# Kernel tuning notes

Hardware: AMD Instinct MI355X
Metric: run time of the kernel (lower is better)

## Reference

```python
import jax, jax.numpy as jnp
import numpy as np

EPS = 1e-12  # matches torch F.normalize eps


def _l2norm(x, axis):
    n = jnp.sqrt(jnp.sum(x * x, axis=axis, keepdims=True))
    return x / jnp.maximum(n, EPS)


def _avg_pool(x, k):
    # x: [B, C, H, W], H and W divisible by k
    B, C, H, W = x.shape
    return x.reshape(B, C, H // k, k, W // k, k).mean(axis=(3, 5))


def setup_inputs() -> dict:
    key = jax.random.key(0)
    k1, k2, k3, k4 = jax.random.split(key, 4)
    B, N, C = 4, 256, 256
    Hp, Wp = 96, 128
    return {
        "q_t": jax.random.normal(k1, (B, N, C), dtype=jnp.float32),
        "f_t": jax.random.normal(k2, (B, Hp * Wp, C), dtype=jnp.float32),
        "w1": jax.random.normal(k3, (16, 4, 3, 3), dtype=jnp.float32) * 0.1,
        "w2": jax.random.normal(k4, (1, 16, 3, 3), dtype=jnp.float32) * 0.1,
        "H_prime": 96,
        "W_prime": 128,
    }


def reference(q_t, f_t, w1, w2, H_prime, W_prime):
    B, N, C = q_t.shape
    qn = _l2norm(q_t, axis=-1)  # [B, N, C]
    # f_t: [B, P, C] -> [B, C, H', W']
    f = f_t.reshape(B, H_prime, W_prime, C).transpose(0, 3, 1, 2)
    cs = []
    for i in range(4):  # pyramid levels, pool kernel 1/2/4/8
        k = 1 << i
        fl = f if k == 1 else _avg_pool(f, k)
        h, w = H_prime // k, W_prime // k
        fln = _l2norm(fl.reshape(B, C, h * w), axis=1)  # normalize over channels
        c = jnp.einsum('bnc,bcp->bnp', qn, fln)  # [B, N, h*w]
        c = c.reshape(B * N, 1, h, w)
        if k > 1:
            # torch bilinear align_corners=False == half-pixel linear resize
            c = jax.image.resize(c, (B * N, 1, H_prime, W_prime), method='linear')
        cs.append(c)
    c = jnp.concatenate(cs, axis=1)  # [B*N, 4, H', W']
    # cnn_corr branch: conv3x3 -> relu -> conv3x3, residual with level-0 corr
    hmid = jax.lax.conv_general_dilated(c, w1, (1, 1), 'SAME')
    hmid = jax.nn.relu(hmid)
    out = jax.lax.conv_general_dilated(hmid, w2, (1, 1), 'SAME') + c[:, 0:1]
    return out.reshape(B, N, H_prime * W_prime)
```

## Files before the change

### kernel.cpp

```cpp
#include <hip/hip_runtime.h>
#include <hip/hip_fp16.h>

#define BB 4
#define NN 256
#define CC 256
#define HH 96
#define WW 128
#define P0 (HH*WW)
#define TOTPOS 16320

#define SH 16
#define SW 64
#define CTH 20
#define CTW 68
#define HMH 18
#define HMW 66

typedef _Float16 f16x4 __attribute__((ext_vector_type(4)));
typedef _Float16 f16x8 __attribute__((ext_vector_type(8)));
typedef _Float16 h2    __attribute__((ext_vector_type(2)));
typedef float    f32x4 __attribute__((ext_vector_type(4)));

#if defined(__has_builtin)
#if __has_builtin(__builtin_amdgcn_fdot2)
#define FDOT2(a,b,c) __builtin_amdgcn_fdot2((a),(b),(c),false)
#endif
#endif
#ifndef FDOT2
#define FDOT2(a,b,c) ((c) + (float)(a)[0]*(float)(b)[0] + (float)(a)[1]*(float)(b)[1])
#endif

union F4U { f16x4 v; uint2 u; };
union F8U { f16x8 v; uint4 u; h2 h[4]; };

__device__ __forceinline__ int hm_swz(int hx) {
    return (hx & 0xC) << 2;
}

__global__ __launch_bounds__(64) void k_prep(const float* __restrict__ w1,
                                             _Float16* __restrict__ bfT) {
    int lane = threadIdx.x;
    int oc = lane & 15, og = lane >> 4;
    f16x8 bf0, bf1;
    #pragma unroll
    for (int e = 0; e < 8; ++e) {
        int k0 = og * 8 + e;
        bf0[e] = (_Float16)w1[oc * 36 + (k0 & 3) * 9 + (k0 >> 2)];
        int k1 = 32 + og * 8 + e;
        int kk1 = k1 >> 2;
        bf1[e] = (kk1 <= 8) ? (_Float16)w1[oc * 36 + (k1 & 3) * 9 + kk1] : (_Float16)0.f;
    }
    *(f16x8*)(bfT + lane * 16)     = bf0;
    *(f16x8*)(bfT + lane * 16 + 8) = bf1;
}

__global__ __launch_bounds__(256) void k_qnorm(const float* __restrict__ q,
                                               _Float16* __restrict__ qn16) {
    int wid = blockIdx.x * 4 + (threadIdx.x >> 6);
    int lane = threadIdx.x & 63;
    const float4* src = (const float4*)(q + (size_t)wid * CC);
    float4 v = src[lane];
    float ss = v.x*v.x + v.y*v.y + v.z*v.z + v.w*v.w;
    #pragma unroll
    for (int off = 32; off > 0; off >>= 1) ss += __shfl_xor(ss, off, 64);
    float inv = 1.0f / fmaxf(sqrtf(ss), 1e-12f);
    f16x4 o;
    o[0] = (_Float16)(v.x*inv); o[1] = (_Float16)(v.y*inv);
    o[2] = (_Float16)(v.z*inv); o[3] = (_Float16)(v.w*inv);
    *(f16x4*)(qn16 + (size_t)wid * CC + lane * 4) = o;
}

__global__ __launch_bounds__(256) void k_pool_norm(const float* __restrict__ f,
                                                   _Float16* __restrict__ flnT) {
    int b = blockIdx.y;
    int gp = blockIdx.x;
    int lvl, pos;
    if (gp < 12288)      { lvl = 0; pos = gp; }
    else if (gp < 15360) { lvl = 1; pos = gp - 12288; }
    else if (gp < 16128) { lvl = 2; pos = gp - 15360; }
    else                 { lvl = 3; pos = gp - 16128; }
    int k = 1 << lvl;
    int wl = WW >> lvl;
    int py = pos / wl, px = pos - py * wl;
    int c = threadIdx.x;
    int iy0 = py * k, ix0 = px * k;
    float sum = 0.f;
    for (int dy = 0; dy < k; ++dy)
        for (int dx = 0; dx < k; ++dx) {
            int ip = (iy0 + dy) * WW + ix0 + dx;
            sum += f[((size_t)b * P0 + ip) * CC + c];
        }
    float val = sum * (1.0f / (float)(k * k));
    float ss = val * val;
    #pragma unroll
    for (int off = 32; off > 0; off >>= 1) ss += __shfl_xor(ss, off, 64);
    __shared__ float red[4];
    __shared__ float s_inv;
    if ((threadIdx.x & 63) == 0) red[threadIdx.x >> 6] = ss;
    __syncthreads();
    if (threadIdx.x == 0) {
        float t = red[0] + red[1] + red[2] + red[3];
        s_inv = 1.0f / fmaxf(sqrtf(t), 1e-12f);
    }
    __syncthreads();
    flnT[((size_t)b * TOTPOS + gp) * CC + c] = (_Float16)(val * s_inv);
}

__global__ __launch_bounds__(256, 4) void k_gemm(const _Float16* __restrict__ qn16,
                                                 const _Float16* __restrict__ flnT,
                                                 float* __restrict__ cws) {
    int b = blockIdx.z;
    int wv = threadIdx.x >> 6, lane = threadIdx.x & 63;
    int m0 = blockIdx.y * 64 + (wv >> 1) * 32;
    int p0 = blockIdx.x * 64 + (wv & 1) * 32;
    int r = lane & 15, og = lane >> 4;

    const f16x8* A0p = (const f16x8*)(qn16 + ((size_t)(b * NN + m0 + r)) * CC) + og;
    const f16x8* A1p = (const f16x8*)(qn16 + ((size_t)(b * NN + m0 + 16 + r)) * CC) + og;
    const f16x8* B0p = (const f16x8*)(flnT + ((size_t)b * TOTPOS + p0 + r) * CC) + og;
    const f16x8* B1p = (const f16x8*)(flnT + ((size_t)b * TOTPOS + p0 + 16 + r) * CC) + og;

    f32x4 acc00 = {0,0,0,0}, acc01 = {0,0,0,0}, acc10 = {0,0,0,0}, acc11 = {0,0,0,0};
    #pragma unroll 4
    for (int ko = 0; ko < 8; ++ko) {
        f16x8 a0 = A0p[ko * 4];
        f16x8 a1 = A1p[ko * 4];
        f16x8 b0 = B0p[ko * 4];
        f16x8 b1 = B1p[ko * 4];
        acc00 = __builtin_amdgcn_mfma_f32_16x16x32_f16(a0, b0, acc00, 0, 0, 0);
        acc01 = __builtin_amdgcn_mfma_f32_16x16x32_f16(a0, b1, acc01, 0, 0, 0);
        acc10 = __builtin_amdgcn_mfma_f32_16x16x32_f16(a1, b0, acc10, 0, 0, 0);
        acc11 = __builtin_amdgcn_mfma_f32_16x16x32_f16(a1, b1, acc11, 0, 0, 0);
    }
    size_t rowBase = (size_t)(b * NN + m0 + og * 4) * TOTPOS;
    #pragma unroll
    for (int rr = 0; rr < 4; ++rr) {
        size_t ro0 = rowBase + (size_t)rr * TOTPOS;
        size_t ro1 = ro0 + (size_t)16 * TOTPOS;
        cws[ro0 + p0 + r]      = acc00[rr];
        cws[ro0 + p0 + 16 + r] = acc01[rr];
        cws[ro1 + p0 + r]      = acc10[rr];
        cws[ro1 + p0 + 16 + r] = acc11[rr];
    }
}

__global__ __launch_bounds__(512, 6) void k_fuse(const float* __restrict__ cws,
                                                 const _Float16* __restrict__ bfT,
                                                 const float* __restrict__ w2,
                                                 float* __restrict__ out) {
    __shared__ _Float16 cT[CTH * CTW * 4];
    __shared__ _Float16 hm[HMH * HMW * 16];
    __shared__ h2 w2h2[72];
    __shared__ int   xt01[3][CTW];
    __shared__ float xttx[3][CTW];
    __shared__ int   yt01[3][CTH];
    __shared__ float ytty[3][CTH];
    int img   = blockIdx.y;
    int strip = blockIdx.x;
    int y0 = (strip >> 1) * SH;
    int x0 = (strip & 1) * SW;
    int tid = threadIdx.x;
    int lane = tid & 63, wv = tid >> 6;
    int oc = lane & 15, og = lane >> 4;
    const float* cb = cws + (size_t)img * TOTPOS;

    if (tid < 72) {
        int tap = tid >> 3, j = tid & 7;
        h2 w; w[0] = (_Float16)w2[(2 * j) * 9 + tap];
        w[1] = (_Float16)w2[(2 * j + 1) * 9 + tap];
        w2h2[tid] = w;
    }
    for (int i = tid; i < 3 * CTW; i += 512) {
        int l = i / CTW + 1, rx = i - (l - 1) * CTW;
        int wl = WW >> l;
        float invk = (l == 1) ? 0.5f : (l == 2) ? 0.25f : 0.125f;
        float fx = ((x0 + rx - 2) + 0.5f) * invk - 0.5f;
        float x0f = floorf(fx);
        int ix = (int)x0f;
        int x1 = min(ix + 1, wl - 1); if (x1 < 0) x1 = 0;
        int xc = min(max(ix, 0), wl - 1);
        xt01[l - 1][rx] = xc | (x1 << 16);
        xttx[l - 1][rx] = fx - x0f;
    }
    if (tid < 3 * CTH) {
        int l = tid / CTH + 1, ry = tid - (l - 1) * CTH;
        int hl = HH >> l;
        float invk = (l == 1) ? 0.5f : (l == 2) ? 0.25f : 0.125f;
        float fy = ((y0 + ry - 2) + 0.5f) * invk - 0.5f;
        float y0f = floorf(fy);
        int iy = (int)y0f;
        int y1 = min(iy + 1, hl - 1); if (y1 < 0) y1 = 0;
        int yc = min(max(iy, 0), hl - 1);
        yt01[l - 1][ry] = yc | (y1 << 16);
        ytty[l - 1][ry] = fy - y0f;
    }

    f16x8 bf0 = *(const f16x8*)(bfT + lane * 16);
    f16x8 bf1 = *(const f16x8*)(bfT + lane * 16 + 8);
    int ofs0, ofs1, ofs8;
    {
        int kk0 = 2 * og,     ky0 = kk0 / 3, kx0 = kk0 - ky0 * 3;
        int kk1 = 2 * og + 1, ky1 = kk1 / 3, kx1 = kk1 - ky1 * 3;
        ofs0 = (ky0 * CTW + kx0 + 1 + oc) * 4;
        ofs1 = (ky1 * CTW + kx1 + 1 + oc) * 4;
        ofs8 = (2 * CTW + 2 + 1 + oc) * 4;
    }
    {
        uint4 z; z.x = z.y = z.z = z.w = 0u;
        uint4* hp = (uint4*)hm;
        for (int i = tid; i < (HMH * HMW * 16 * 2) / 16; i += 512) hp[i] = z;
    }
    __syncthreads();

    for (int i = tid; i < CTH * CTW; i += 512) {
        int ry = i / CTW, rx = i - ry * CTW;
        int gy = y0 + ry - 2, gx = x0 + rx - 2;
        f16x4 vv = {(_Float16)0.f, (_Float16)0.f, (_Float16)0.f, (_Float16)0.f};
        if ((unsigned)gy < HH && (unsigned)gx < WW) {
            vv[0] = (_Float16)cb[gy * WW + gx];
            #pragma unroll
            for (int l = 1; l < 4; ++l) {
                int wl = WW >> l;
                int lvlOff = (l == 1) ? 12288 : (l == 2) ? 15360 : 16128;
                int p01 = xt01[l - 1][rx];
                float tx = xttx[l - 1][rx];
                int q01 = yt01[l - 1][ry];
                float ty = ytty[l - 1][ry];
                int xa = p01 & 0xFFFF, xb = p01 >> 16;
                int ya = q01 & 0xFFFF, yb = q01 >> 16;
                const float* r0 = cb + lvlOff + ya * wl;
                const float* r1 = cb + lvlOff + yb * wl;
                float v00 = r0[xa], v01 = r0[xb];
                float v10 = r1[xa], v11 = r1[xb];
                float top = v00 + tx * (v01 - v00);
                float bot = v10 + tx * (v11 - v10);
                vv[l] = (_Float16)(top + ty * (bot - top));
            }
        }
        *(f16x4*)&cT[i * 4] = vv;
    }
    __syncthreads();

    for (int it = 0; it < 12; ++it) {
        int t = it * 8 + wv;
        if (t >= 90) break;
        int hyr = t / 5, xg = t - hyr * 5;
        if ((unsigned)(y0 + hyr - 1) >= (unsigned)HH) continue;
        int xb = (xg < 4) ? xg * 16 - 1 : 49;
        int base = (hyr * CTW + xb) * 4;
        F4U a00, a01, a8;
        a00.v = *(const f16x4*)&cT[base + ofs0];
        a01.v = *(const f16x4*)&cT[base + ofs1];
        a8.v  = *(const f16x4*)&cT[base + ofs8];
        F8U A0, A1;
        A0.u.x = a00.u.x; A0.u.y = a00.u.y; A0.u.z = a01.u.x; A0.u.w = a01.u.y;
        A1.u.x = a8.u.x;  A1.u.y = a8.u.y;  A1.u.z = a8.u.x;  A1.u.w = a8.u.y;
        f32x4 acc = {0.f, 0.f, 0.f, 0.f};
        acc = __builtin_amdgcn_mfma_f32_16x16x32_f16(A0.v, bf0, acc, 0, 0, 0);
        acc = __builtin_amdgcn_mfma_f32_16x16x32_f16(A1.v, bf1, acc, 0, 0, 0);
        int hxb = xb + og * 4 + 1;
        #pragma unroll
        for (int r = 0; r < 4; ++r) {
            int hx = hxb + r;
            int imgx = x0 + hx - 1;
            bool st = ((unsigned)imgx < (unsigned)WW) && (xg < 4 || hx >= 64);
            if (st) {
                int byt = ((hyr * HMW + hx) * 32 + oc * 2) ^ hm_swz(hx);
                *(_Float16*)((char*)hm + byt) = (_Float16)fmaxf(acc[r], 0.f);
            }
        }
    }
    __syncthreads();

    int row = tid >> 5, x2 = (tid & 31) * 2;
    int colof[4][2];
    #pragma unroll
    for (int c4 = 0; c4 < 4; ++c4) {
        int hx = x2 + c4;
        int sw = hm_swz(hx);
        colof[c4][0] = (hx * 32) ^ sw;
        colof[c4][1] = (hx * 32 + 16) ^ sw;
    }
    float a2[2] = {0.f, 0.f};
    #pragma unroll
    for (int r = 0; r < 3; ++r) {
        int rowb = (row + r) * (HMW * 32);
        h2 wrow[3][8];
        #pragma unroll
        for (int kx = 0; kx < 3; ++kx)
            #pragma unroll
            for (int j = 0; j < 8; ++j) wrow[kx][j] = w2h2[(r * 3 + kx) * 8 + j];
        F8U d[4][2];
        #pragma unroll
        for (int c4 = 0; c4 < 4; ++c4) {
            d[c4][0].v = *(const f16x8*)((const char*)hm + (rowb + colof[c4][0]));
            d[c4][1].v = *(const f16x8*)((const char*)hm + (rowb + colof[c4][1]));
        }
        #pragma unroll
        for (int q = 0; q < 2; ++q)
            #pragma unroll
            for (int kx = 0; kx < 3; ++kx) {
                #pragma unroll
                for (int j = 0; j < 4; ++j) {
                    a2[q] = FDOT2(d[q + kx][0].h[j], wrow[kx][j], a2[q]);
                    a2[q] = FDOT2(d[q + kx][1].h[j], wrow[kx][j + 4], a2[q]);
                }
            }
    }
    int gy = y0 + row, gx = x0 + x2;
    const float2 res = *(const float2*)&cb[gy * WW + gx];
    float2 o;
    o.x = a2[0] + res.x; o.y = a2[1] + res.y;
    *(float2*)&out[(size_t)img * P0 + gy * WW + gx] = o;
}

extern "C" void kernel_launch(void* const* d_in, const int* in_sizes, int n_in,
                              void* d_out, int out_size, void* d_ws, size_t ws_size,
                              hipStream_t stream) {
    const float* q  = (const float*)d_in[0];
    const float* f  = (const float*)d_in[1];
    const float* w1 = (const float*)d_in[2];
    const float* w2 = (const float*)d_in[3];
    float* out = (float*)d_out;

    float* cws = (float*)d_ws;
    _Float16* flnT = (_Float16*)(cws + (size_t)BB * NN * TOTPOS);
    _Float16* qn16 = flnT + (size_t)BB * TOTPOS * CC;
    _Float16* bfT  = qn16 + (size_t)BB * NN * CC;

    hipLaunchKernelGGL(k_prep, dim3(1), dim3(64), 0, stream, w1, bfT);
    hipLaunchKernelGGL(k_qnorm, dim3(BB * NN / 4), dim3(256), 0, stream, q, qn16);
    hipLaunchKernelGGL(k_pool_norm, dim3(TOTPOS, BB), dim3(256), 0, stream, f, flnT);
    hipLaunchKernelGGL(k_gemm, dim3(255, 4, BB), dim3(256), 0, stream, qn16, flnT, cws);
    hipLaunchKernelGGL(k_fuse, dim3(12, BB * NN), dim3(512), 0, stream, cws, bfT, w2, out);
}
```

Baseline: 345.9 us.

## Store correlation in fp16 and precompute bilinear upsampled levels in separate kernel

The GEMM now writes the correlation workspace in fp16 instead of fp32, halving that write traffic. A new kernel performs the bilinear upsampling of the three pooled levels once per image into three full-resolution fp16 buffers, so the fused conv kernel loads four values per pixel instead of recomputing the interpolation with gathers in every overlapping tile. The residual is taken from the shared-memory tile rather than reloaded from global memory. The trade-off is three extra full-resolution buffers (about 3x 25MB) that must be written and read back, plus an extra launch, and fp16 rounding of the residual term.

```diff
diff --git a/kernel.cpp b/kernel.cpp
--- a/kernel.cpp
+++ b/kernel.cpp
@@ -108,7 +108,7 @@
 
 __global__ __launch_bounds__(256, 4) void k_gemm(const _Float16* __restrict__ qn16,
                                                  const _Float16* __restrict__ flnT,
-                                                 float* __restrict__ cws) {
+                                                 _Float16* __restrict__ cws16) {
     int b = blockIdx.z;
     int wv = threadIdx.x >> 6, lane = threadIdx.x & 63;
     int m0 = blockIdx.y * 64 + (wv >> 1) * 32;
@@ -137,24 +137,57 @@
     for (int rr = 0; rr < 4; ++rr) {
         size_t ro0 = rowBase + (size_t)rr * TOTPOS;
         size_t ro1 = ro0 + (size_t)16 * TOTPOS;
-        cws[ro0 + p0 + r]      = acc00[rr];
-        cws[ro0 + p0 + 16 + r] = acc01[rr];
-        cws[ro1 + p0 + r]      = acc10[rr];
-        cws[ro1 + p0 + 16 + r] = acc11[rr];
-    }
-}
-
-__global__ __launch_bounds__(512, 6) void k_fuse(const float* __restrict__ cws,
+        cws16[ro0 + p0 + r]      = (_Float16)acc00[rr];
+        cws16[ro0 + p0 + 16 + r] = (_Float16)acc01[rr];
+        cws16[ro1 + p0 + r]      = (_Float16)acc10[rr];
+        cws16[ro1 + p0 + 16 + r] = (_Float16)acc11[rr];
+    }
+}
+
+__global__ __launch_bounds__(256) void k_upsample(const _Float16* __restrict__ cws16,
+                                                  _Float16* __restrict__ cu1,
+                                                  _Float16* __restrict__ cu2,
+                                                  _Float16* __restrict__ cu3) {
+    int img = blockIdx.y;
+    int p = blockIdx.x * 256 + threadIdx.x;
+    int y = p >> 7, x = p & 127;
+    const _Float16* cb = cws16 + (size_t)img * TOTPOS;
+    _Float16 r[3];
+    #pragma unroll
+    for (int l = 1; l < 4; ++l) {
+        int hl = HH >> l, wl = WW >> l;
+        int lvlOff = (l == 1) ? 12288 : (l == 2) ? 15360 : 16128;
+        float invk = (l == 1) ? 0.5f : (l == 2) ? 0.25f : 0.125f;
+        float fy = (y + 0.5f) * invk - 0.5f;
+        float fx = (x + 0.5f) * invk - 0.5f;
+        float y0f = floorf(fy), x0f = floorf(fx);
+        float ty = fy - y0f, tx = fx - x0f;
+        int iy = (int)y0f, ix = (int)x0f;
+        int y1 = min(iy + 1, hl - 1);
+        iy = min(max(iy, 0), hl - 1);
+        int x1 = min(ix + 1, wl - 1);
+        ix = min(max(ix, 0), wl - 1);
+        const _Float16* base = cb + lvlOff;
+        float v00 = (float)base[iy * wl + ix], v01 = (float)base[iy * wl + x1];
+        float v10 = (float)base[y1 * wl + ix], v11 = (float)base[y1 * wl + x1];
+        float top = v00 + tx * (v01 - v00);
+        float bot = v10 + tx * (v11 - v10);
+        r[l - 1] = (_Float16)(top + ty * (bot - top));
+    }
+    size_t o = (size_t)img * P0 + p;
+    cu1[o] = r[0]; cu2[o] = r[1]; cu3[o] = r[2];
+}
+
+__global__ __launch_bounds__(512, 6) void k_fuse(const _Float16* __restrict__ cws16,
+                                                 const _Float16* __restrict__ cu1,
+                                                 const _Float16* __restrict__ cu2,
+                                                 const _Float16* __restrict__ cu3,
                                                  const _Float16* __restrict__ bfT,
                                                  const float* __restrict__ w2,
                                                  float* __restrict__ out) {
     __shared__ _Float16 cT[CTH * CTW * 4];
     __shared__ _Float16 hm[HMH * HMW * 16];
     __shared__ h2 w2h2[72];
-    __shared__ int   xt01[3][CTW];
-    __shared__ float xttx[3][CTW];
-    __shared__ int   yt01[3][CTH];
-    __shared__ float ytty[3][CTH];
     int img   = blockIdx.y;
     int strip = blockIdx.x;
     int y0 = (strip >> 1) * SH;
@@ -162,37 +195,14 @@
     int tid = threadIdx.x;
     int lane = tid & 63, wv = tid >> 6;
     int oc = lane & 15, og = lane >> 4;
-    const float* cb = cws + (size_t)img * TOTPOS;
+    const _Float16* cb16 = cws16 + (size_t)img * TOTPOS;
+    size_t ib = (size_t)img * P0;
 
     if (tid < 72) {
         int tap = tid >> 3, j = tid & 7;
         h2 w; w[0] = (_Float16)w2[(2 * j) * 9 + tap];
         w[1] = (_Float16)w2[(2 * j + 1) * 9 + tap];
         w2h2[tid] = w;
-    }
-    for (int i = tid; i < 3 * CTW; i += 512) {
-        int l = i / CTW + 1, rx = i - (l - 1) * CTW;
-        int wl = WW >> l;
-        float invk = (l == 1) ? 0.5f : (l == 2) ? 0.25f : 0.125f;
-        float fx = ((x0 + rx - 2) + 0.5f) * invk - 0.5f;
-        float x0f = floorf(fx);
-        int ix = (int)x0f;
-        int x1 = min(ix + 1, wl - 1); if (x1 < 0) x1 = 0;
-        int xc = min(max(ix, 0), wl - 1);
-        xt01[l - 1][rx] = xc | (x1 << 16);
-        xttx[l - 1][rx] = fx - x0f;
-    }
-    if (tid < 3 * CTH) {
-        int l = tid / CTH + 1, ry = tid - (l - 1) * CTH;
-        int hl = HH >> l;
-        float invk = (l == 1) ? 0.5f : (l == 2) ? 0.25f : 0.125f;
-        float fy = ((y0 + ry - 2) + 0.5f) * invk - 0.5f;
-        float y0f = floorf(fy);
-        int iy = (int)y0f;
-        int y1 = min(iy + 1, hl - 1); if (y1 < 0) y1 = 0;
-        int yc = min(max(iy, 0), hl - 1);
-        yt01[l - 1][ry] = yc | (y1 << 16);
-        ytty[l - 1][ry] = fy - y0f;
     }
 
     f16x8 bf0 = *(const f16x8*)(bfT + lane * 16);
@@ -210,32 +220,16 @@
         uint4* hp = (uint4*)hm;
         for (int i = tid; i < (HMH * HMW * 16 * 2) / 16; i += 512) hp[i] = z;
     }
-    __syncthreads();
-
     for (int i = tid; i < CTH * CTW; i += 512) {
         int ry = i / CTW, rx = i - ry * CTW;
         int gy = y0 + ry - 2, gx = x0 + rx - 2;
         f16x4 vv = {(_Float16)0.f, (_Float16)0.f, (_Float16)0.f, (_Float16)0.f};
         if ((unsigned)gy < HH && (unsigned)gx < WW) {
-            vv[0] = (_Float16)cb[gy * WW + gx];
-            #pragma unroll
-            for (int l = 1; l < 4; ++l) {
-                int wl = WW >> l;
-                int lvlOff = (l == 1) ? 12288 : (l == 2) ? 15360 : 16128;
-                int p01 = xt01[l - 1][rx];
-                float tx = xttx[l - 1][rx];
-                int q01 = yt01[l - 1][ry];
-                float ty = ytty[l - 1][ry];
-                int xa = p01 & 0xFFFF, xb = p01 >> 16;
-                int ya = q01 & 0xFFFF, yb = q01 >> 16;
-                const float* r0 = cb + lvlOff + ya * wl;
-                const float* r1 = cb + lvlOff + yb * wl;
-                float v00 = r0[xa], v01 = r0[xb];
-                float v10 = r1[xa], v11 = r1[xb];
-                float top = v00 + tx * (v01 - v00);
-                float bot = v10 + tx * (v11 - v10);
-                vv[l] = (_Float16)(top + ty * (bot - top));
-            }
+            int gp = gy * WW + gx;
+            vv[0] = cb16[gp];
+            vv[1] = cu1[ib + gp];
+            vv[2] = cu2[ib + gp];
+            vv[3] = cu3[ib + gp];
         }
         *(f16x4*)&cT[i * 4] = vv;
     }
@@ -308,9 +302,10 @@
             }
     }
     int gy = y0 + row, gx = x0 + x2;
-    const float2 res = *(const float2*)&cb[gy * WW + gx];
+    float r0 = (float)cT[((row + 2) * CTW + (x2 + 2)) * 4];
+    float r1 = (float)cT[((row + 2) * CTW + (x2 + 3)) * 4];
     float2 o;
-    o.x = a2[0] + res.x; o.y = a2[1] + res.y;
+    o.x = a2[0] + r0; o.y = a2[1] + r1;
     *(float2*)&out[(size_t)img * P0 + gy * WW + gx] = o;
 }
 
@@ -323,14 +318,20 @@
     const float* w2 = (const float*)d_in[3];
     float* out = (float*)d_out;
 
-    float* cws = (float*)d_ws;
-    _Float16* flnT = (_Float16*)(cws + (size_t)BB * NN * TOTPOS);
+    _Float16* wsh  = (_Float16*)d_ws;
+    _Float16* cws16 = wsh;
+    _Float16* cu1  = cws16 + (size_t)BB * NN * TOTPOS;
+    _Float16* cu2  = cu1 + (size_t)BB * NN * P0;
+    _Float16* cu3  = cu2 + (size_t)BB * NN * P0;
+    _Float16* flnT = cu3 + (size_t)BB * NN * P0;
     _Float16* qn16 = flnT + (size_t)BB * TOTPOS * CC;
     _Float16* bfT  = qn16 + (size_t)BB * NN * CC;
 
     hipLaunchKernelGGL(k_prep, dim3(1), dim3(64), 0, stream, w1, bfT);
     hipLaunchKernelGGL(k_qnorm, dim3(BB * NN / 4), dim3(256), 0, stream, q, qn16);
     hipLaunchKernelGGL(k_pool_norm, dim3(TOTPOS, BB), dim3(256), 0, stream, f, flnT);
-    hipLaunchKernelGGL(k_gemm, dim3(255, 4, BB), dim3(256), 0, stream, qn16, flnT, cws);
-    hipLaunchKernelGGL(k_fuse, dim3(12, BB * NN), dim3(512), 0, stream, cws, bfT, w2, out);
-}
+    hipLaunchKernelGGL(k_gemm, dim3(255, 4, BB), dim3(256), 0, stream, qn16, flnT, cws16);
+    hipLaunchKernelGGL(k_upsample, dim3(48, BB * NN), dim3(256), 0, stream, cws16, cu1, cu2, cu3);
+    hipLaunchKernelGGL(k_fuse, dim3(12, BB * NN), dim3(512), 0, stream,
+                       cws16, cu1, cu2, cu3, bfT, w2, out);
+}
```

Result: slower. 362.1 us (+4.7%).

## Store correlation workspace in fp16 and trim conv epilogue overheads

Applied to the files above, without the earlier changes.

The GEMM now writes the correlation volume as fp16 instead of fp32, so the write traffic and the gathered reads in the fuse kernel are halved. The residual add now reads the level-0 value from the shared-memory tile instead of global memory. The hidden-layer store branches are specialised to drop per-element bounds checks, and the w2 weights are loaded as 16-byte vectors. The cost is extra fp16 rounding of the correlation before bilinear interpolation and in the residual path, which may reduce accuracy.

```diff
diff --git a/kernel.cpp b/kernel.cpp
--- a/kernel.cpp
+++ b/kernel.cpp
@@ -108,7 +108,7 @@
 
 __global__ __launch_bounds__(256, 4) void k_gemm(const _Float16* __restrict__ qn16,
                                                  const _Float16* __restrict__ flnT,
-                                                 float* __restrict__ cws) {
+                                                 _Float16* __restrict__ cws16) {
     int b = blockIdx.z;
     int wv = threadIdx.x >> 6, lane = threadIdx.x & 63;
     int m0 = blockIdx.y * 64 + (wv >> 1) * 32;
@@ -137,14 +137,14 @@
     for (int rr = 0; rr < 4; ++rr) {
         size_t ro0 = rowBase + (size_t)rr * TOTPOS;
         size_t ro1 = ro0 + (size_t)16 * TOTPOS;
-        cws[ro0 + p0 + r]      = acc00[rr];
-        cws[ro0 + p0 + 16 + r] = acc01[rr];
-        cws[ro1 + p0 + r]      = acc10[rr];
-        cws[ro1 + p0 + 16 + r] = acc11[rr];
-    }
-}
-
-__global__ __launch_bounds__(512, 6) void k_fuse(const float* __restrict__ cws,
+        cws16[ro0 + p0 + r]      = (_Float16)acc00[rr];
+        cws16[ro0 + p0 + 16 + r] = (_Float16)acc01[rr];
+        cws16[ro1 + p0 + r]      = (_Float16)acc10[rr];
+        cws16[ro1 + p0 + 16 + r] = (_Float16)acc11[rr];
+    }
+}
+
+__global__ __launch_bounds__(512, 6) void k_fuse(const _Float16* __restrict__ cws16,
                                                  const _Float16* __restrict__ bfT,
                                                  const float* __restrict__ w2,
                                                  float* __restrict__ out) {
@@ -162,7 +162,7 @@
     int tid = threadIdx.x;
     int lane = tid & 63, wv = tid >> 6;
     int oc = lane & 15, og = lane >> 4;
-    const float* cb = cws + (size_t)img * TOTPOS;
+    const _Float16* cb16 = cws16 + (size_t)img * TOTPOS;
 
     if (tid < 72) {
         int tap = tid >> 3, j = tid & 7;
@@ -217,7 +217,7 @@
         int gy = y0 + ry - 2, gx = x0 + rx - 2;
         f16x4 vv = {(_Float16)0.f, (_Float16)0.f, (_Float16)0.f, (_Float16)0.f};
         if ((unsigned)gy < HH && (unsigned)gx < WW) {
-            vv[0] = (_Float16)cb[gy * WW + gx];
+            vv[0] = cb16[gy * WW + gx];
             #pragma unroll
             for (int l = 1; l < 4; ++l) {
                 int wl = WW >> l;
@@ -228,10 +228,10 @@
                 float ty = ytty[l - 1][ry];
                 int xa = p01 & 0xFFFF, xb = p01 >> 16;
                 int ya = q01 & 0xFFFF, yb = q01 >> 16;
-                const float* r0 = cb + lvlOff + ya * wl;
-                const float* r1 = cb + lvlOff + yb * wl;
-                float v00 = r0[xa], v01 = r0[xb];
-                float v10 = r1[xa], v11 = r1[xb];
+                const _Float16* r0 = cb16 + lvlOff + ya * wl;
+                const _Float16* r1 = cb16 + lvlOff + yb * wl;
+                float v00 = (float)r0[xa], v01 = (float)r0[xb];
+                float v10 = (float)r1[xa], v11 = (float)r1[xb];
                 float top = v00 + tx * (v01 - v00);
                 float bot = v10 + tx * (v11 - v10);
                 vv[l] = (_Float16)(top + ty * (bot - top));
@@ -259,14 +259,33 @@
         acc = __builtin_amdgcn_mfma_f32_16x16x32_f16(A0.v, bf0, acc, 0, 0, 0);
         acc = __builtin_amdgcn_mfma_f32_16x16x32_f16(A1.v, bf1, acc, 0, 0, 0);
         int hxb = xb + og * 4 + 1;
-        #pragma unroll
-        for (int r = 0; r < 4; ++r) {
-            int hx = hxb + r;
-            int imgx = x0 + hx - 1;
-            bool st = ((unsigned)imgx < (unsigned)WW) && (xg < 4 || hx >= 64);
-            if (st) {
-                int byt = ((hyr * HMW + hx) * 32 + oc * 2) ^ hm_swz(hx);
-                *(_Float16*)((char*)hm + byt) = (_Float16)fmaxf(acc[r], 0.f);
+        if (xg < 4) {
+            if (x0 == 0 && xg == 0) {
+                #pragma unroll
+                for (int r = 0; r < 4; ++r) {
+                    int hx = hxb + r;
+                    if (hx > 0) {
+                        int byt = ((hyr * HMW + hx) * 32 + oc * 2) ^ hm_swz(hx);
+                        *(_Float16*)((char*)hm + byt) = (_Float16)fmaxf(acc[r], 0.f);
+                    }
+                }
+            } else {
+                #pragma unroll
+                for (int r = 0; r < 4; ++r) {
+                    int hx = hxb + r;
+                    int byt = ((hyr * HMW + hx) * 32 + oc * 2) ^ hm_swz(hx);
+                    *(_Float16*)((char*)hm + byt) = (_Float16)fmaxf(acc[r], 0.f);
+                }
+            }
+        } else {
+            #pragma unroll
+            for (int r = 0; r < 4; ++r) {
+                int hx = hxb + r;
+                int imgx = x0 + hx - 1;
+                if (hx >= 64 && (unsigned)imgx < (unsigned)WW) {
+                    int byt = ((hyr * HMW + hx) * 32 + oc * 2) ^ hm_swz(hx);
+                    *(_Float16*)((char*)hm + byt) = (_Float16)fmaxf(acc[r], 0.f);
+                }
             }
         }
     }
@@ -285,11 +304,12 @@
     #pragma unroll
     for (int r = 0; r < 3; ++r) {
         int rowb = (row + r) * (HMW * 32);
-        h2 wrow[3][8];
-        #pragma unroll
-        for (int kx = 0; kx < 3; ++kx)
+        F8U ww[6];
+        {
+            const f16x8* wp = (const f16x8*)(w2h2 + r * 24);
             #pragma unroll
-            for (int j = 0; j < 8; ++j) wrow[kx][j] = w2h2[(r * 3 + kx) * 8 + j];
+            for (int j = 0; j < 6; ++j) ww[j].v = wp[j];
+        }
         F8U d[4][2];
         #pragma unroll
         for (int c4 = 0; c4 < 4; ++c4) {
@@ -302,15 +322,18 @@
             for (int kx = 0; kx < 3; ++kx) {
                 #pragma unroll
                 for (int j = 0; j < 4; ++j) {
-                    a2[q] = FDOT2(d[q + kx][0].h[j], wrow[kx][j], a2[q]);
-                    a2[q] = FDOT2(d[q + kx][1].h[j], wrow[kx][j + 4], a2[q]);
+                    int fi0 = kx * 8 + j;
+                    int fi1 = kx * 8 + j + 4;
+                    a2[q] = FDOT2(d[q + kx][0].h[j], ww[fi0 >> 2].h[fi0 & 3], a2[q]);
+                    a2[q] = FDOT2(d[q + kx][1].h[j], ww[fi1 >> 2].h[fi1 & 3], a2[q]);
                 }
             }
     }
     int gy = y0 + row, gx = x0 + x2;
-    const float2 res = *(const float2*)&cb[gy * WW + gx];
+    float r0 = (float)cT[((row + 2) * CTW + (x2 + 2)) * 4];
+    float r1 = (float)cT[((row + 2) * CTW + (x2 + 3)) * 4];
     float2 o;
-    o.x = a2[0] + res.x; o.y = a2[1] + res.y;
+    o.x = a2[0] + r0; o.y = a2[1] + r1;
     *(float2*)&out[(size_t)img * P0 + gy * WW + gx] = o;
 }
 
@@ -323,14 +346,15 @@
     const float* w2 = (const float*)d_in[3];
     float* out = (float*)d_out;
 
-    float* cws = (float*)d_ws;
-    _Float16* flnT = (_Float16*)(cws + (size_t)BB * NN * TOTPOS);
-    _Float16* qn16 = flnT + (size_t)BB * TOTPOS * CC;
-    _Float16* bfT  = qn16 + (size_t)BB * NN * CC;
+    _Float16* wsh   = (_Float16*)d_ws;
+    _Float16* cws16 = wsh;
+    _Float16* flnT  = cws16 + (size_t)BB * NN * TOTPOS;
+    _Float16* qn16  = flnT + (size_t)BB * TOTPOS * CC;
+    _Float16* bfT   = qn16 + (size_t)BB * NN * CC;
 
     hipLaunchKernelGGL(k_prep, dim3(1), dim3(64), 0, stream, w1, bfT);
     hipLaunchKernelGGL(k_qnorm, dim3(BB * NN / 4), dim3(256), 0, stream, q, qn16);
     hipLaunchKernelGGL(k_pool_norm, dim3(TOTPOS, BB), dim3(256), 0, stream, f, flnT);
-    hipLaunchKernelGGL(k_gemm, dim3(255, 4, BB), dim3(256), 0, stream, qn16, flnT, cws);
-    hipLaunchKernelGGL(k_fuse, dim3(12, BB * NN), dim3(512), 0, stream, cws, bfT, w2, out);
-}
+    hipLaunchKernelGGL(k_gemm, dim3(255, 4, BB), dim3(256), 0, stream, qn16, flnT, cws16);
+    hipLaunchKernelGGL(k_fuse, dim3(12, BB * NN), dim3(512), 0, stream, cws16, bfT, w2, out);
+}
```

Result: slower. 360.1 us (+4.1%).

## Compute all pyramid levels per 8x8 tile in one pass over features

Applied to the files above, without the earlier changes.

The pooling/normalization kernel now gives each block an 8x8 spatial tile. The block loads the tile into shared memory once as fp16, builds the 2x2, 4x4 and 8x8 pooled levels hierarchically, and computes per-position channel norms cooperatively before writing all levels. Before, every level re-read the full fp32 feature map, so the input was read about four times; now it is read once, and the launch drops from 16320 tiny blocks to 192 per batch. The trade-off is about 45 KB of shared memory per block, which limits occupancy. Storing raw features in fp16 before pooling and normalizing also adds slight rounding differences.

```diff
diff --git a/kernel.cpp b/kernel.cpp
--- a/kernel.cpp
+++ b/kernel.cpp
@@ -72,38 +72,99 @@
 
 __global__ __launch_bounds__(256) void k_pool_norm(const float* __restrict__ f,
                                                    _Float16* __restrict__ flnT) {
+    __shared__ _Float16 vals[64][258];
+    __shared__ _Float16 pooled[21][258];
+    __shared__ float part_ss[256];
+    __shared__ float inv_norm[85];
     int b = blockIdx.y;
-    int gp = blockIdx.x;
-    int lvl, pos;
-    if (gp < 12288)      { lvl = 0; pos = gp; }
-    else if (gp < 15360) { lvl = 1; pos = gp - 12288; }
-    else if (gp < 16128) { lvl = 2; pos = gp - 15360; }
-    else                 { lvl = 3; pos = gp - 16128; }
-    int k = 1 << lvl;
-    int wl = WW >> lvl;
-    int py = pos / wl, px = pos - py * wl;
+    int tile = blockIdx.x;
+    int ty = tile >> 4, tx = tile & 15;
     int c = threadIdx.x;
-    int iy0 = py * k, ix0 = px * k;
-    float sum = 0.f;
-    for (int dy = 0; dy < k; ++dy)
-        for (int dx = 0; dx < k; ++dx) {
-            int ip = (iy0 + dy) * WW + ix0 + dx;
-            sum += f[((size_t)b * P0 + ip) * CC + c];
+
+    const float* fb = f + ((size_t)b * P0) * CC + c;
+    #pragma unroll 4
+    for (int p = 0; p < 64; ++p) {
+        int py = p >> 3, px = p & 7;
+        int ip = (ty * 8 + py) * WW + tx * 8 + px;
+        vals[p][c] = (_Float16)fb[(size_t)ip * CC];
+    }
+    __syncthreads();
+
+    #pragma unroll
+    for (int p1 = 0; p1 < 16; ++p1) {
+        int py = p1 >> 2, px = p1 & 3;
+        float s = (float)vals[(2*py)*8 + 2*px][c]     + (float)vals[(2*py)*8 + 2*px + 1][c]
+                + (float)vals[(2*py+1)*8 + 2*px][c]   + (float)vals[(2*py+1)*8 + 2*px + 1][c];
+        pooled[p1][c] = (_Float16)(s * 0.25f);
+    }
+    #pragma unroll
+    for (int p2 = 0; p2 < 4; ++p2) {
+        int py = p2 >> 1, px = p2 & 1;
+        float s = (float)pooled[(2*py)*4 + 2*px][c]   + (float)pooled[(2*py)*4 + 2*px + 1][c]
+                + (float)pooled[(2*py+1)*4 + 2*px][c] + (float)pooled[(2*py+1)*4 + 2*px + 1][c];
+        pooled[16 + p2][c] = (_Float16)(s * 0.25f);
+    }
+    {
+        float s = (float)pooled[16][c] + (float)pooled[17][c]
+                + (float)pooled[18][c] + (float)pooled[19][c];
+        pooled[20][c] = (_Float16)(s * 0.25f);
+    }
+    __syncthreads();
+
+    {
+        int pos = c >> 2, part = c & 3;
+        float ss = 0.f;
+        const _Float16* vp = &vals[pos][part * 64];
+        #pragma unroll 8
+        for (int j = 0; j < 64; ++j) { float v = (float)vp[j]; ss += v * v; }
+        part_ss[c] = ss;
+    }
+    __syncthreads();
+    if (c < 64) {
+        float t = part_ss[4*c] + part_ss[4*c+1] + part_ss[4*c+2] + part_ss[4*c+3];
+        inv_norm[c] = 1.0f / fmaxf(sqrtf(t), 1e-12f);
+    }
+    __syncthreads();
+    {
+        int pos = c >> 2, part = c & 3;
+        float ss = 0.f;
+        if (pos < 21) {
+            const _Float16* vp = &pooled[pos][part * 64];
+            #pragma unroll 8
+            for (int j = 0; j < 64; ++j) { float v = (float)vp[j]; ss += v * v; }
         }
-    float val = sum * (1.0f / (float)(k * k));
-    float ss = val * val;
-    #pragma unroll
-    for (int off = 32; off > 0; off >>= 1) ss += __shfl_xor(ss, off, 64);
-    __shared__ float red[4];
-    __shared__ float s_inv;
-    if ((threadIdx.x & 63) == 0) red[threadIdx.x >> 6] = ss;
-    __syncthreads();
-    if (threadIdx.x == 0) {
-        float t = red[0] + red[1] + red[2] + red[3];
-        s_inv = 1.0f / fmaxf(sqrtf(t), 1e-12f);
-    }
-    __syncthreads();
-    flnT[((size_t)b * TOTPOS + gp) * CC + c] = (_Float16)(val * s_inv);
+        part_ss[c] = ss;
+    }
+    __syncthreads();
+    if (c < 21) {
+        float t = part_ss[4*c] + part_ss[4*c+1] + part_ss[4*c+2] + part_ss[4*c+3];
+        inv_norm[64 + c] = 1.0f / fmaxf(sqrtf(t), 1e-12f);
+    }
+    __syncthreads();
+
+    size_t base = (size_t)b * TOTPOS;
+    #pragma unroll 4
+    for (int p = 0; p < 64; ++p) {
+        int py = p >> 3, px = p & 7;
+        int gp = (ty * 8 + py) * WW + tx * 8 + px;
+        flnT[(base + gp) * CC + c] = (_Float16)((float)vals[p][c] * inv_norm[p]);
+    }
+    #pragma unroll
+    for (int p1 = 0; p1 < 16; ++p1) {
+        int py = p1 >> 2, px = p1 & 3;
+        int gp = 12288 + (ty * 4 + py) * 64 + tx * 4 + px;
+        flnT[(base + gp) * CC + c] = (_Float16)((float)pooled[p1][c] * inv_norm[64 + p1]);
+    }
+    #pragma unroll
+    for (int p2 = 0; p2 < 4; ++p2) {
+        int py = p2 >> 1, px = p2 & 1;
+        int gp = 15360 + (ty * 2 + py) * 32 + tx * 2 + px;
+        flnT[(base + gp) * CC + c] = (_Float16)((float)pooled[16 + p2][c] * inv_norm[80 + p2]);
+    }
+    {
+        int gp = 16128 + ty * 16 + tx;
+        flnT[(base + gp) * CC + c] = (_Float16)((float)pooled[20][c] * inv_norm[84]);
+    }
 }
 
 __global__ __launch_bounds__(256, 4) void k_gemm(const _Float16* __restrict__ qn16,
@@ -330,7 +391,7 @@
 
     hipLaunchKernelGGL(k_prep, dim3(1), dim3(64), 0, stream, w1, bfT);
     hipLaunchKernelGGL(k_qnorm, dim3(BB * NN / 4), dim3(256), 0, stream, q, qn16);
-    hipLaunchKernelGGL(k_pool_norm, dim3(TOTPOS, BB), dim3(256), 0, stream, f, flnT);
+    hipLaunchKernelGGL(k_pool_norm, dim3(192, BB), dim3(256), 0, stream, f, flnT);
     hipLaunchKernelGGL(k_gemm, dim3(255, 4, BB), dim3(256), 0, stream, qn16, flnT, cws);
     hipLaunchKernelGGL(k_fuse, dim3(12, BB * NN), dim3(512), 0, stream, cws, bfT, w2, out);
 }
```

After: 286.7 us (median of 2 runs). -17.1%, faster.
